# Optimization experiments

Hardware: AMD Instinct MI355X
Metric: run time of the kernel (lower is better)

## Reference

```python
import jax, jax.numpy as jnp
import numpy as np

SEQ = 10; NCH = 7; NNODES = 10; GH = 32; HEADS = 4; LH = 64; NUSERS = 1000

def _edges():
    e = []
    for i in range(4):
        e += [[i, 7], [7, i]]
    for i in range(4, 7):
        e += [[i, 8], [8, i]]
    e += [[7, 8], [8, 7], [7, 9], [9, 7], [8, 9], [9, 8]]
    a = np.array(e, dtype=np.int32)
    return a[:, 0], a[:, 1]

_SRC, _DST = _edges()

def gat_conv(x, W, att_src, att_dst, bias, concat):
    # x: [B,N,Fin], W: [Fin,H,C], att_*: [H,C]. PyG GATConv: adds self-loops, leaky_relu(0.2), edge-softmax by dst.
    src = jnp.concatenate([jnp.asarray(_SRC), jnp.arange(NNODES, dtype=jnp.int32)])
    dst = jnp.concatenate([jnp.asarray(_DST), jnp.arange(NNODES, dtype=jnp.int32)])
    xh = jnp.einsum('bnf,fhc->bnhc', x, W)            # [B,N,H,C]
    a_s = (xh * att_src).sum(-1)                       # [B,N,H]
    a_d = (xh * att_dst).sum(-1)
    e = jax.nn.leaky_relu(a_s[:, src] + a_d[:, dst], 0.2)  # [B,E,H]
    B = x.shape[0]
    m = jnp.full((B, NNODES, e.shape[-1]), -jnp.inf, e.dtype).at[:, dst].max(e)
    p = jnp.exp(e - m[:, dst])
    den = jnp.zeros((B, NNODES, e.shape[-1]), e.dtype).at[:, dst].add(p)
    alpha = p / den[:, dst]                            # softmax over incoming edges
    out = jnp.zeros(xh.shape, xh.dtype).at[:, dst].add(alpha[..., None] * xh[:, src])
    out = out.reshape(B, NNODES, -1) if concat else out.mean(axis=2)
    return out + bias

def graph_conv(x, W_rel, b_rel, W_root):
    # PyG GraphConv(aggr='add'): lin_rel(sum_{j->i} x_j) + lin_root(x_i); no self-loops.
    src = jnp.asarray(_SRC); dst = jnp.asarray(_DST)
    agg = jnp.zeros_like(x).at[:, dst].add(x[:, src])
    return agg @ W_rel + b_rel + x @ W_root

def lstm_dir(x, Wih, Whh, b):
    B, T, _ = x.shape
    H = Whh.shape[1]
    xw = jnp.einsum('btd,gd->btg', x, Wih) + b         # precompute input projections [B,T,4H]
    def step(carry, xt):
        h, c = carry
        g = xt + h @ Whh.T
        i, f, gg, o = jnp.split(g, 4, -1)
        c = jax.nn.sigmoid(f) * c + jax.nn.sigmoid(i) * jnp.tanh(gg)
        h = jax.nn.sigmoid(o) * jnp.tanh(c)
        return (h, c), h
    z = jnp.zeros((B, H), x.dtype)
    _, hs = jax.lax.scan(step, (z, z), xw.transpose(1, 0, 2))
    return hs.transpose(1, 0, 2)

def bilstm(x, Wf, Uf, bf, Wb, Ub, bb):
    fwd = lstm_dir(x, Wf, Uf, bf)
    bwd = lstm_dir(x[:, ::-1], Wb, Ub, bb)[:, ::-1]
    return jnp.concatenate([fwd, bwd], -1)

def self_attn(O, Wa, ba):
    Q = jnp.tanh(O @ Wa.T + ba)
    a = jax.nn.softmax(jnp.einsum('bqh,bkh->bqk', Q, O), axis=-1)
    return jnp.einsum('bqk,bkh->bqh', a, O)

_SPECS = {
    'ga1_W': (SEQ, HEADS, GH), 'ga1_as': (HEADS, GH), 'ga1_ad': (HEADS, GH), 'ga1_b': (HEADS * GH,),
    'ga2_W': (HEADS * GH, 1, SEQ), 'ga2_as': (1, SEQ), 'ga2_ad': (1, SEQ), 'ga2_b': (SEQ,),
    'gp1_Wrel': (SEQ, GH), 'gp1_Wroot': (SEQ, GH), 'gp1_b': (GH,),
    'gp2_Wrel': (GH, SEQ), 'gp2_Wroot': (GH, SEQ), 'gp2_b': (SEQ,),
    'l1f_Wih': (4 * LH, 3 * NCH), 'l1f_Whh': (4 * LH, LH), 'l1f_b': (4 * LH,),
    'l1b_Wih': (4 * LH, 3 * NCH), 'l1b_Whh': (4 * LH, LH), 'l1b_b': (4 * LH,),
    'l2f_Wih': (4 * LH, 2 * LH), 'l2f_Whh': (4 * LH, LH), 'l2f_b': (4 * LH,),
    'l2b_Wih': (4 * LH, 2 * LH), 'l2b_Whh': (4 * LH, LH), 'l2b_b': (4 * LH,),
    'a1_Wa': (2 * LH, 2 * LH), 'a1_ba': (2 * LH,),
    'a2_Wa': (2 * LH, 2 * LH), 'a2_ba': (2 * LH,),
    'fc_W': (NUSERS, 2 * LH), 'fc_b': (NUSERS,),
}

def setup_inputs() -> dict:
    key = jax.random.key(0)
    B = 32768
    keys = jax.random.split(key, len(_SPECS) + 1)
    inp = {'M': jax.random.normal(keys[0], (B, NCH, SEQ), dtype=jnp.float32)}
    for k, (name, shp) in zip(keys[1:], _SPECS.items()):
        inp[name] = (jax.random.normal(k, shp, dtype=jnp.float32) * 0.1)
    return inp

def reference(M, ga1_W, ga1_as, ga1_ad, ga1_b, ga2_W, ga2_as, ga2_ad, ga2_b,
              gp1_Wrel, gp1_Wroot, gp1_b, gp2_Wrel, gp2_Wroot, gp2_b,
              l1f_Wih, l1f_Whh, l1f_b, l1b_Wih, l1b_Whh, l1b_b,
              l2f_Wih, l2f_Whh, l2f_b, l2b_Wih, l2b_Whh, l2b_b,
              a1_Wa, a1_ba, a2_Wa, a2_ba, fc_W, fc_b):
    B = M.shape[0]
    pad = jnp.zeros((B, NNODES - NCH, SEQ), M.dtype)
    nf = jnp.concatenate([M, pad], axis=1)             # [B,10,10]
    h = jax.nn.relu(gat_conv(nf, ga1_W, ga1_as, ga1_ad, ga1_b, True))
    Mp = gat_conv(h, ga2_W, ga2_as, ga2_ad, ga2_b, False)[:, :NCH]
    g = jax.nn.relu(graph_conv(nf, gp1_Wrel, gp1_b, gp1_Wroot))
    bfeat = graph_conv(g, gp2_Wrel, gp2_b, gp2_Wroot)[:, :NCH]
    x = jnp.concatenate([M.transpose(0, 2, 1), Mp.transpose(0, 2, 1), bfeat.transpose(0, 2, 1)], axis=2)
    x = bilstm(x, l1f_Wih, l1f_Whh, l1f_b, l1b_Wih, l1b_Whh, l1b_b)
    x = self_attn(x, a1_Wa, a1_ba)
    x = bilstm(x, l2f_Wih, l2f_Whh, l2f_b, l2b_Wih, l2b_Whh, l2b_b)
    x = self_attn(x, a2_Wa, a2_ba)
    x = x.mean(axis=1)
    return x @ fc_W.T + fc_b
```

## Files before the change

kernel.cpp:

```cpp
#include <hip/hip_runtime.h>
#include <hip/hip_bf16.h>
#include <cstdint>


#define NCH 7
#define SEQ 10
#define NN  10

__constant__ int c_src[20] = {0,7,1,7,2,7,3,7,4,8,5,8,6,8,7,8,7,9,8,9};
__constant__ int c_dst[20] = {7,0,7,1,7,2,7,3,8,4,8,5,8,6,8,7,9,7,9,8};
__constant__ int c_in_start[11] = {0,2,4,6,8,10,12,14,21,27,30};
__constant__ int c_in_edge[30] = {1,20, 3,21, 5,22, 7,23, 9,24, 11,25, 13,26,
                                  0,2,4,6,15,17,27,
                                  8,10,12,14,19,28,
                                  16,18,29};
__constant__ int c_gin_start[11] = {0,1,2,3,4,5,6,7,13,18,20};
__constant__ int c_gin_src[20] = {7,7,7,7,8,8,8, 0,1,2,3,8,9, 4,5,6,7,9, 7,8};

__device__ __forceinline__ float fsig(float x){ return 1.f/(1.f + __expf(-x)); }
__device__ __forceinline__ float ftanh(float x){ return 1.f - 2.f/(__expf(2.f*x) + 1.f); }

typedef _Float16 h2v __attribute__((ext_vector_type(2)));
typedef _Float16 f16x4 __attribute__((ext_vector_type(4)));
typedef float    f32x4 __attribute__((ext_vector_type(4)));

#if defined(__has_builtin)
#if __has_builtin(__builtin_amdgcn_fdot2)
#define HAS_FDOT2 1
#endif
#endif

__device__ __forceinline__ float d2(uint32_t a, uint32_t b, float c){
#ifdef HAS_FDOT2
    return __builtin_amdgcn_fdot2(__builtin_bit_cast(h2v, a),
                                  __builtin_bit_cast(h2v, b), c, false);
#else
    union { uint32_t u; _Float16 h[2]; } ua, ub;
    ua.u = a; ub.u = b;
    return c + (float)ua.h[0]*(float)ub.h[0] + (float)ua.h[1]*(float)ub.h[1];
#endif
}

__device__ __forceinline__ f32x4 mfma16(f16x4 a, f16x4 b, f32x4 c){
    return __builtin_amdgcn_mfma_f32_16x16x16f16(a, b, c, 0, 0, 0);
}
__device__ __forceinline__ f16x4 ld4h(const _Float16* p){
    return __builtin_bit_cast(f16x4, *(const uint2*)(p));
}
__device__ __forceinline__ f16x4 ld4hg(const uint32_t* p){
    return __builtin_bit_cast(f16x4, *(const uint2*)(p));
}
__device__ __forceinline__ uint32_t pk2(float a, float b){
    union { _Float16 h[2]; uint32_t u; } x;
    x.h[0] = (_Float16)a; x.h[1] = (_Float16)b; return x.u;
}
__device__ __forceinline__ float2 upk2(uint32_t u){
    union { uint32_t u; _Float16 h[2]; } x; x.u = u;
    return make_float2((float)x.h[0], (float)x.h[1]);
}
#define SBAR() __builtin_amdgcn_sched_barrier(0)

#define IH1O 0
#define HH1O 8192
#define IH2O 24576
#define HH2O 57344
#define WA1O 73728
#define WA2O 81920
#define WPK_TOTAL 90112

__global__ __launch_bounds__(256) void prep_kernel(
    const float* __restrict__ w1f, const float* __restrict__ w1b,
    const float* __restrict__ h1f, const float* __restrict__ h1b,
    const float* __restrict__ w2f, const float* __restrict__ w2b,
    const float* __restrict__ h2f, const float* __restrict__ h2b,
    const float* __restrict__ wa1, const float* __restrict__ wa2,
    uint32_t* __restrict__ wpk)
{
    int i = blockIdx.x * 256 + threadIdx.x;
    if (i >= WPK_TOTAL) return;
    float v0, v1;
    if (i < 73728) {
        const float *sa, *sb; int K, NKT, base;
        if (i < 8192)       { base = 0;     NKT = 2; K = 21;  sa = w1f; sb = w1b; }
        else if (i < 24576) { base = 8192;  NKT = 4; K = 64;  sa = h1f; sb = h1b; }
        else if (i < 57344) { base = 24576; NKT = 8; K = 128; sa = w2f; sb = w2b; }
        else                { base = 57344; NKT = 4; K = 64;  sa = h2f; sb = h2b; }
        int local = i - base;
        int dsz = 16 * NKT * 128;
        const float* src = sa;
        if (local >= dsz) { src = sb; local -= dsz; }
        int entry = local >> 7;
        int lane  = (local & 127) >> 1;
        int j     = local & 1;
        int tau = entry / NKT, kt = entry - tau * NKT;
        int row = 16 * tau + (lane & 15);
        int kb  = kt * 16 + 4 * (lane >> 4) + 2 * j;
        v0 = (kb     < K) ? src[row * K + kb]     : 0.f;
        v1 = (kb + 1 < K) ? src[row * K + kb + 1] : 0.f;
    } else {
        int local = i - 73728;
        const float* src = wa1;
        if (local >= 8192) { src = wa2; local -= 8192; }
        int row = local >> 6, p = local & 63;
        int d0 = 2 * p;
        v0 = src[row * 128 + d0];
        v1 = src[row * 128 + d0 + 1];
    }
    union { _Float16 h[2]; uint32_t u; } x;
    x.h[0] = (_Float16)v0; x.h[1] = (_Float16)v1;
    wpk[i] = x.u;
}

__global__ __launch_bounds__(64) void graph_kernel(
    const float* __restrict__ M,
    const float* __restrict__ W1, const float* __restrict__ as1,
    const float* __restrict__ ad1, const float* __restrict__ b1,
    const float* __restrict__ W2, const float* __restrict__ as2,
    const float* __restrict__ ad2, const float* __restrict__ b2,
    const float* __restrict__ gWrel1, const float* __restrict__ gWroot1,
    const float* __restrict__ gb1,
    const float* __restrict__ gWrel2, const float* __restrict__ gWroot2,
    const float* __restrict__ gb2,
    float* __restrict__ xseq)
{
    const int b = blockIdx.x;
    const int tid = threadIdx.x;

    __shared__ float    s_nf[10][10];
    __shared__ uint32_t s_xhp[10][64];
    __shared__ uint32_t s_hp[10][64];
    __shared__ uint32_t s_w2p[10][64];
    __shared__ uint32_t s_a1p[64], s_d1p[64];
    __shared__ float s_as[10][4], s_ad[10][4];
    __shared__ float s_al[30][4];
    __shared__ float s_xh2[10][10];
    __shared__ float s_as2[10], s_ad2[10];
    __shared__ float s_al2[30];
    __shared__ float s_mp[10][10];
    __shared__ float s_agg[10][10];
    __shared__ float s_g[10][33];
    __shared__ float s_gagg[10][33];
    __shared__ float s_bf[10][10];

    const float* Mb = M + (size_t)b * 70;
    for (int i = tid; i < 100; i += 64) {
        int n = i / 10, f = i - n * 10;
        s_nf[n][f] = (n < 7) ? Mb[n * 10 + f] : 0.f;
    }
    s_a1p[tid] = pk2(as1[2 * tid], as1[2 * tid + 1]);
    s_d1p[tid] = pk2(ad1[2 * tid], ad1[2 * tid + 1]);
    for (int i = tid; i < 640; i += 64) {
        int c = i >> 6, j = i & 63;
        s_w2p[c][j] = pk2(W2[(2 * j) * 10 + c], W2[(2 * j + 1) * 10 + c]);
    }
    float2 w1r[10];
    #pragma unroll
    for (int f = 0; f < 10; f++)
        w1r[f] = *(const float2*)(W1 + f * 128 + 2 * tid);
    SBAR();

    #pragma unroll
    for (int n = 0; n < 10; n++) {
        float a0 = 0.f, a1 = 0.f;
        #pragma unroll
        for (int f = 0; f < 10; f++) {
            float x = s_nf[n][f];
            a0 += x * w1r[f].x; a1 += x * w1r[f].y;
        }
        s_xhp[n][tid] = pk2(a0, a1);
    }
    SBAR();

    if (tid < 40) {
        int n = tid >> 2, h = tid & 3;
        float va = 0.f, vd = 0.f;
        #pragma unroll
        for (int cp = 0; cp < 16; cp++) {
            uint32_t x = s_xhp[n][h * 16 + cp];
            va = d2(x, s_a1p[h * 16 + cp], va);
            vd = d2(x, s_d1p[h * 16 + cp], vd);
        }
        s_as[n][h] = va; s_ad[n][h] = vd;
    }
    SBAR();

    for (int i = tid; i < 120; i += 64) {
        int e = i >> 2, h = i & 3;
        int sn = (e < 20) ? c_src[e] : e - 20;
        int dn = (e < 20) ? c_dst[e] : e - 20;
        float v = s_as[sn][h] + s_ad[dn][h];
        s_al[e][h] = (v >= 0.f) ? v : 0.2f * v;
    }
    SBAR();

    if (tid < 40) {
        int n = tid >> 2, h = tid & 3;
        int st = c_in_start[n], en = c_in_start[n+1];
        float m = -1e30f;
        for (int j = st; j < en; j++) m = fmaxf(m, s_al[c_in_edge[j]][h]);
        float den = 0.f;
        for (int j = st; j < en; j++) den += __expf(s_al[c_in_edge[j]][h] - m);
        float inv = 1.f / den;
        for (int j = st; j < en; j++) {
            int e = c_in_edge[j];
            s_al[e][h] = __expf(s_al[e][h] - m) * inv;
        }
    }
    SBAR();

    for (int i = tid; i < 640; i += 64) {
        int n = i >> 6, p = i & 63;
        int h = p >> 4;
        int st = c_in_start[n], en = c_in_start[n+1];
        float2 bb = *(const float2*)(b1 + 2 * p);
        float o0 = bb.x, o1 = bb.y;
        for (int j = st; j < en; j++) {
            int e = c_in_edge[j];
            int sn = (e < 20) ? c_src[e] : e - 20;
            float al = s_al[e][h];
            float2 xf = upk2(s_xhp[sn][p]);
            o0 += al * xf.x; o1 += al * xf.y;
        }
        s_hp[n][p] = pk2(fmaxf(o0, 0.f), fmaxf(o1, 0.f));
    }
    SBAR();

    for (int i = tid; i < 100; i += 64) {
        int n = i / 10, c = i - (i / 10) * 10;
        float a = 0.f;
        #pragma unroll 16
        for (int j = 0; j < 64; j++)
            a = d2(s_hp[n][j], s_w2p[c][j], a);
        s_xh2[n][c] = a;
    }
    SBAR();

    if (tid < 20) {
        int n = (tid < 10) ? tid : tid - 10;
        const float* av = (tid < 10) ? as2 : ad2;
        float v = 0.f;
        #pragma unroll
        for (int c = 0; c < 10; c++) v += s_xh2[n][c] * av[c];
        if (tid < 10) s_as2[n] = v; else s_ad2[n] = v;
    }
    SBAR();
    if (tid < 30) {
        int e = tid;
        int sn = (e < 20) ? c_src[e] : e - 20;
        int dn = (e < 20) ? c_dst[e] : e - 20;
        float v = s_as2[sn] + s_ad2[dn];
        s_al2[e] = (v >= 0.f) ? v : 0.2f * v;
    }
    SBAR();
    if (tid < 10) {
        int st = c_in_start[tid], en = c_in_start[tid+1];
        float m = -1e30f;
        for (int j = st; j < en; j++) m = fmaxf(m, s_al2[c_in_edge[j]]);
        float den = 0.f;
        for (int j = st; j < en; j++) den += __expf(s_al2[c_in_edge[j]] - m);
        float inv = 1.f / den;
        for (int j = st; j < en; j++) s_al2[c_in_edge[j]] = __expf(s_al2[c_in_edge[j]] - m) * inv;
    }
    SBAR();
    for (int i = tid; i < 100; i += 64) {
        int n = i / 10, c = i - (i / 10) * 10;
        int st = c_in_start[n], en = c_in_start[n+1];
        float o = b2[c];
        for (int j = st; j < en; j++) {
            int e = c_in_edge[j];
            int sn = (e < 20) ? c_src[e] : e - 20;
            o += s_al2[e] * s_xh2[sn][c];
        }
        s_mp[n][c] = o;
    }
    SBAR();

    for (int i = tid; i < 100; i += 64) {
        int n = i / 10, f = i - (i / 10) * 10;
        int st = c_gin_start[n], en = c_gin_start[n+1];
        float a = 0.f;
        for (int j = st; j < en; j++) a += s_nf[c_gin_src[j]][f];
        s_agg[n][f] = a;
    }
    SBAR();
    for (int i = tid; i < 320; i += 64) {
        int n = i >> 5, c = i & 31;
        float v = gb1[c];
        #pragma unroll
        for (int f = 0; f < 10; f++)
            v += s_agg[n][f] * gWrel1[f*32 + c] + s_nf[n][f] * gWroot1[f*32 + c];
        s_g[n][c] = fmaxf(v, 0.f);
    }
    SBAR();
    for (int i = tid; i < 320; i += 64) {
        int n = i >> 5, c = i & 31;
        int st = c_gin_start[n], en = c_gin_start[n+1];
        float a = 0.f;
        for (int j = st; j < en; j++) a += s_g[c_gin_src[j]][c];
        s_gagg[n][c] = a;
    }
    SBAR();
    for (int i = tid; i < 100; i += 64) {
        int n = i / 10, c = i - (i / 10) * 10;
        float v = gb2[c];
        #pragma unroll
        for (int f = 0; f < 32; f++)
            v += s_gagg[n][f] * gWrel2[f*10 + c] + s_g[n][f] * gWroot2[f*10 + c];
        s_bf[n][c] = v;
    }
    SBAR();

    float* xo = xseq + (size_t)b * 210;
    for (int i = tid; i < 210; i += 64) {
        int t = i / 21, k = i - (i / 21) * 21;
        float v;
        if (k < 7)       v = s_nf[k][t];
        else if (k < 14) v = s_mp[k - 7][t];
        else             v = s_bf[k - 14][t];
        xo[i] = v;
    }
}


template<int L>
__device__ __forceinline__ void rec_layer(
    const uint32_t* __restrict__ wpk,
    const float* __restrict__ bf, const float* __restrict__ bb,
    uint32_t* __restrict__ sR1, uint32_t* __restrict__ sO2,
    uint32_t* __restrict__ sH, int w, int l)
{
    constexpr int NKT = (L == 1) ? 2 : 8;
    const uint32_t* bih = wpk + ((L == 1) ? IH1O : IH2O);
    const uint32_t* bhh = wpk + ((L == 1) ? HH1O : HH2O);
    const int dir = w >> 1;
    const int ub  = (w & 1) * 2;
    bih += dir * 16 * NKT * 128;
    bhh += dir * 16 * 4 * 128;
    const float* bias = dir ? bb : bf;
    const int ln = l & 15, lg = l >> 4;
    const int arow = l & 7, asub = 4 * lg;
    float bv[2][4];
    #pragma unroll
    for (int up = 0; up < 2; ++up)
        #pragma unroll
        for (int g = 0; g < 4; ++g)
            bv[up][g] = bias[64 * g + 16 * (ub + up) + ln];
    float cs[2][4] = {{0.f,0.f,0.f,0.f},{0.f,0.f,0.f,0.f}};
    const _Float16* Axh = (const _Float16*)sR1;
    _Float16* Hh  = (_Float16*)sH;
    _Float16* O2h = (_Float16*)sO2;
    for (int ss = 0; ss < 10; ++ss) {
        const int t = dir ? 9 - ss : ss;
        const int cur = ss & 1;
        f16x4 ax[NKT];
        #pragma unroll
        for (int kt = 0; kt < NKT; ++kt) {
            const int fo = (L == 1) ? (arow * 360 + t * 36 + kt * 16 + asub)
                                    : (arow * 1360 + t * 136 + kt * 16 + asub);
            ax[kt] = ld4h(Axh + fo);
        }
        f16x4 ah[4];
        #pragma unroll
        for (int kt = 0; kt < 4; ++kt)
            ah[kt] = ld4h(Hh + ((dir * 2 + cur) * 8 + arow) * 72 + kt * 16 + asub);
        #pragma unroll
        for (int up = 0; up < 2; ++up) {
            const int v = ub + up;
            f32x4 G[4];
            #pragma unroll
            for (int g = 0; g < 4; ++g) {
                const int tau = 4 * g + v;
                f32x4 c = { bv[up][g], bv[up][g], bv[up][g], bv[up][g] };
                #pragma unroll
                for (int kt = 0; kt < NKT; ++kt)
                    c = mfma16(ax[kt], ld4hg(bih + (tau * NKT + kt) * 128 + 2 * l), c);
                #pragma unroll
                for (int kt = 0; kt < 4; ++kt)
                    c = mfma16(ah[kt], ld4hg(bhh + (tau * 4 + kt) * 128 + 2 * l), c);
                G[g] = c;
            }
            if (l < 32) {
                #pragma unroll
                for (int r = 0; r < 4; ++r) {
                    const int s = asub + r;
                    const float ig = fsig(G[0][r]), fg = fsig(G[1][r]);
                    const float gg = ftanh(G[2][r]), og = fsig(G[3][r]);
                    const float c2 = fg * cs[up][r] + ig * gg;
                    cs[up][r] = c2;
                    const float hv = og * ftanh(c2);
                    const int u = 16 * v + ln;
                    Hh[((dir * 2 + (1 - cur)) * 8 + s) * 72 + u] = (_Float16)hv;
                    O2h[s * 1360 + t * 136 + dir * 64 + u] = (_Float16)hv;
                }
            }
        }
        __syncthreads();
    }
}

__device__ __forceinline__ void attn_one(
    const uint32_t* __restrict__ wa, const float* __restrict__ ba,
    uint32_t* __restrict__ sR1, const uint32_t* __restrict__ sO2,
    float* __restrict__ sSC, int l, int s, float* __restrict__ outg)
{
    const uint32_t* O2s = sO2 + s * 680;
    uint32_t* Q2s = sR1 + s * 680;
    float* sc = sSC + s * 104;

    float qa0[10], qa1[10];
    {
        float b0 = ba[l], b1 = ba[64 + l];
        #pragma unroll
        for (int t = 0; t < 10; t++) { qa0[t] = b0; qa1[t] = b1; }
    }
    #pragma unroll 4
    for (int c = 0; c < 16; c++) {
        uint4 w0 = *(const uint4*)(wa + l * 64 + c * 4);
        uint4 w1 = *(const uint4*)(wa + (64 + l) * 64 + c * 4);
        #pragma unroll
        for (int t = 0; t < 10; t++) {
            uint4 o = *(const uint4*)(O2s + t * 68 + c * 4);
            qa0[t] = d2(w0.w, o.w, d2(w0.z, o.z, d2(w0.y, o.y, d2(w0.x, o.x, qa0[t]))));
            qa1[t] = d2(w1.w, o.w, d2(w1.z, o.z, d2(w1.y, o.y, d2(w1.x, o.x, qa1[t]))));
        }
    }
    _Float16* q2h = (_Float16*)Q2s;
    #pragma unroll
    for (int t = 0; t < 10; t++) {
        q2h[t * 136 + l]      = (_Float16)ftanh(qa0[t]);
        q2h[t * 136 + 64 + l] = (_Float16)ftanh(qa1[t]);
    }
    #pragma unroll
    for (int r = 0; r < 2; r++) {
        int idx = l + r * 64;
        if (idx < 100) {
            int q = idx / 10, k = idx - 10 * q;
            float sv = 0.f;
            #pragma unroll
            for (int m = 0; m < 16; m++) {
                uint4 a = *(const uint4*)(Q2s + q * 68 + m * 4);
                uint4 b = *(const uint4*)(O2s + k * 68 + m * 4);
                sv = d2(a.w, b.w, d2(a.z, b.z, d2(a.y, b.y, d2(a.x, b.x, sv))));
            }
            sc[idx] = sv;
        }
    }
    if (l < 10) {
        float m = -1e30f;
        #pragma unroll
        for (int k = 0; k < 10; k++) m = fmaxf(m, sc[l * 10 + k]);
        float den = 0.f, e[10];
        #pragma unroll
        for (int k = 0; k < 10; k++) { e[k] = __expf(sc[l * 10 + k] - m); den += e[k]; }
        float inv = 1.f / den;
        #pragma unroll
        for (int k = 0; k < 10; k++) sc[l * 10 + k] = e[k] * inv;
    }
    float of0[10], of1[10];
    {
        const _Float16* o2h = (const _Float16*)O2s;
        #pragma unroll
        for (int k = 0; k < 10; k++) {
            of0[k] = (float)o2h[k * 136 + l];
            of1[k] = (float)o2h[k * 136 + 64 + l];
        }
    }
    float pa0[10], pa1[10];
    #pragma unroll
    for (int t = 0; t < 10; t++) { pa0[t] = 0.f; pa1[t] = 0.f; }
    #pragma unroll
    for (int k = 0; k < 10; k++) {
        float o0 = of0[k], o1 = of1[k];
        #pragma unroll
        for (int t = 0; t < 10; t++) {
            float sv = sc[t * 10 + k];
            pa0[t] += sv * o0; pa1[t] += sv * o1;
        }
    }
    if (outg) {
        float s0 = 0.f, s1 = 0.f;
        #pragma unroll
        for (int t = 0; t < 10; t++) { s0 += pa0[t]; s1 += pa1[t]; }
        outg[l] = s0 * 0.1f; outg[64 + l] = s1 * 0.1f;
    } else {
        _Float16* a2h = (_Float16*)Q2s;
        #pragma unroll
        for (int t = 0; t < 10; t++) {
            a2h[t * 136 + l]      = (_Float16)pa0[t];
            a2h[t * 136 + 64 + l] = (_Float16)pa1[t];
        }
    }
}

__global__ __launch_bounds__(256) void seq_kernel(
    const float* __restrict__ xseq, const uint32_t* __restrict__ wpk,
    const float* __restrict__ b1f, const float* __restrict__ b1b,
    const float* __restrict__ b2f, const float* __restrict__ b2b,
    const float* __restrict__ ba1, const float* __restrict__ ba2,
    float* __restrict__ xbar)
{
    __shared__ __align__(16) uint32_t sR1[8 * 680];
    __shared__ __align__(16) uint32_t sO2[8 * 680];
    __shared__ __align__(16) float    sSC[8 * 104];
    __shared__ __align__(16) uint32_t sH[1152];
    const int tid = threadIdx.x;
    const int w = tid >> 6, l = tid & 63;
    const int b0 = blockIdx.x * 8;

    {
        _Float16* xh = (_Float16*)sR1;
        const float* xs = xseq + (size_t)b0 * 210;
        for (int i = tid; i < 2880; i += 256) {
            int s = i / 360, r = i - s * 360;
            int t = r / 36, k = r - t * 36;
            float v = (k < 21) ? xs[s * 210 + t * 21 + k] : 0.f;
            xh[s * 360 + t * 36 + k] = (_Float16)v;
        }
    }
    for (int i = tid; i < 1152; i += 256) sH[i] = 0;
    __syncthreads();

    rec_layer<1>(wpk, b1f, b1b, sR1, sO2, sH, w, l);

    for (int smp = 0; smp < 2; ++smp)
        attn_one(wpk + WA1O, ba1, sR1, sO2, sSC, l, 2 * w + smp, nullptr);
    __syncthreads();
    for (int i = tid; i < 1152; i += 256) sH[i] = 0;
    __syncthreads();

    rec_layer<2>(wpk, b2f, b2b, sR1, sO2, sH, w, l);

    for (int smp = 0; smp < 2; ++smp) {
        int s = 2 * w + smp;
        attn_one(wpk + WA2O, ba2, sR1, sO2, sSC, l, s,
                 xbar + (size_t)(b0 + s) * 128);
    }
}

__global__ __launch_bounds__(256) void fc_kernel(
    const float* __restrict__ xbar, const float* __restrict__ W,
    const float* __restrict__ fb, float* __restrict__ out, int B)
{
    __shared__ __align__(16) float s_xb[64 * 132];
    const int tid = threadIdx.x;
    const int b0 = blockIdx.y * 64;
    const int u0 = blockIdx.x * 64;

    for (int i = tid; i < 64 * 128; i += 256) {
        int s = i >> 7, k = i & 127;
        int bb = b0 + s;
        s_xb[s * 132 + k] = (bb < B) ? xbar[(size_t)bb * 128 + k] : 0.f;
    }
    __syncthreads();

    const int tx = tid & 15, ty = tid >> 4;
    float acc[4][4] = {};
    for (int k = 0; k < 128; k += 4) {
        float4 wv[4], xv[4];
        #pragma unroll
        for (int j = 0; j < 4; j++) {
            int u = u0 + tx + 16 * j;
            int uc = (u < 1000) ? u : 999;
            wv[j] = *(const float4*)(W + (size_t)uc * 128 + k);
        }
        #pragma unroll
        for (int si = 0; si < 4; si++) {
            int s = ty + 16 * si;
            xv[si] = *(const float4*)(s_xb + s * 132 + k);
        }
        #pragma unroll
        for (int j = 0; j < 4; j++)
            #pragma unroll
            for (int si = 0; si < 4; si++)
                acc[j][si] += wv[j].x*xv[si].x + wv[j].y*xv[si].y
                            + wv[j].z*xv[si].z + wv[j].w*xv[si].w;
    }
    #pragma unroll
    for (int j = 0; j < 4; j++) {
        int u = u0 + tx + 16 * j;
        if (u < 1000) {
            float bb = fb[u];
            #pragma unroll
            for (int si = 0; si < 4; si++) {
                int bsm = b0 + ty + 16 * si;
                if (bsm < B) out[(size_t)bsm * 1000 + u] = acc[j][si] + bb;
            }
        }
    }
}

extern "C" void kernel_launch(void* const* d_in, const int* in_sizes, int n_in,
                              void* d_out, int out_size, void* d_ws, size_t ws_size,
                              hipStream_t stream)
{
    const float* M       = (const float*)d_in[0];
    const float* ga1_W   = (const float*)d_in[1];
    const float* ga1_as  = (const float*)d_in[2];
    const float* ga1_ad  = (const float*)d_in[3];
    const float* ga1_b   = (const float*)d_in[4];
    const float* ga2_W   = (const float*)d_in[5];
    const float* ga2_as  = (const float*)d_in[6];
    const float* ga2_ad  = (const float*)d_in[7];
    const float* ga2_b   = (const float*)d_in[8];
    const float* gp1_Wrel  = (const float*)d_in[9];
    const float* gp1_Wroot = (const float*)d_in[10];
    const float* gp1_b     = (const float*)d_in[11];
    const float* gp2_Wrel  = (const float*)d_in[12];
    const float* gp2_Wroot = (const float*)d_in[13];
    const float* gp2_b     = (const float*)d_in[14];
    const float* l1f_Wih = (const float*)d_in[15];
    const float* l1f_Whh = (const float*)d_in[16];
    const float* l1f_b   = (const float*)d_in[17];
    const float* l1b_Wih = (const float*)d_in[18];
    const float* l1b_Whh = (const float*)d_in[19];
    const float* l1b_b   = (const float*)d_in[20];
    const float* l2f_Wih = (const float*)d_in[21];
    const float* l2f_Whh = (const float*)d_in[22];
    const float* l2f_b   = (const float*)d_in[23];
    const float* l2b_Wih = (const float*)d_in[24];
    const float* l2b_Whh = (const float*)d_in[25];
    const float* l2b_b   = (const float*)d_in[26];
    const float* a1_Wa   = (const float*)d_in[27];
    const float* a1_ba   = (const float*)d_in[28];
    const float* a2_Wa   = (const float*)d_in[29];
    const float* a2_ba   = (const float*)d_in[30];
    const float* fc_W    = (const float*)d_in[31];
    const float* fc_b    = (const float*)d_in[32];

    const int B = in_sizes[0] / 70;

    float* xseq = (float*)d_ws;
    float* xbar = (float*)((char*)d_ws + (size_t)B * 210 * 4);
    uint32_t* wpk = (uint32_t*)((char*)d_ws + (size_t)B * 210 * 4
                                            + (size_t)B * 128 * 4);

    prep_kernel<<<(WPK_TOTAL + 255) / 256, 256, 0, stream>>>(
        l1f_Wih, l1b_Wih, l1f_Whh, l1b_Whh,
        l2f_Wih, l2b_Wih, l2f_Whh, l2b_Whh,
        a1_Wa, a2_Wa, wpk);

    graph_kernel<<<B, 64, 0, stream>>>(M,
        ga1_W, ga1_as, ga1_ad, ga1_b,
        ga2_W, ga2_as, ga2_ad, ga2_b,
        gp1_Wrel, gp1_Wroot, gp1_b,
        gp2_Wrel, gp2_Wroot, gp2_b,
        xseq);

    seq_kernel<<<B / 8, 256, 0, stream>>>(xseq, wpk,
        l1f_b, l1b_b, l2f_b, l2b_b, a1_ba, a2_ba, xbar);

    dim3 fgrid((1000 + 63) / 64, (B + 63) / 64);
    fc_kernel<<<fgrid, 256, 0, stream>>>(xbar, fc_W, fc_b, (float*)d_out, B);
}
```

Before: 2.408 ms.

## Process four samples per block in graph kernel with shared-memory staged weights

The graph kernel now runs 256-thread blocks where each 64-lane wave handles one batch sample, using a per-wave workspace struct in LDS. Weights, biases and graph topology tables are loaded once per block into shared memory instead of per-sample global or constant reads. This is meant to cut redundant weight loads and launch/scheduling overhead from many tiny blocks. It increases LDS use per block and assumes the batch size divides by four.

```diff
diff --git a/kernel.cpp b/kernel.cpp
--- a/kernel.cpp
+++ b/kernel.cpp
@@ -111,7 +111,22 @@
     wpk[i] = x.u;
 }
 
-__global__ __launch_bounds__(64) void graph_kernel(
+struct GWk {
+    float    nf[10][10];
+    uint32_t xhp[10][64];
+    uint32_t hp[10][64];
+    float    as_[10][4], ad_[10][4];
+    float    al[30][4];
+    float    xh2[10][10];
+    float    as2[10], ad2[10], al2[30];
+    float    mp[10][10];
+    float    agg[10][10];
+    float    g[10][33];
+    float    gagg[10][33];
+    float    bf[10][10];
+};
+
+__global__ __launch_bounds__(256) void graph_kernel(
     const float* __restrict__ M,
     const float* __restrict__ W1, const float* __restrict__ as1,
     const float* __restrict__ ad1, const float* __restrict__ b1,
@@ -123,40 +138,55 @@
     const float* __restrict__ gb2,
     float* __restrict__ xseq)
 {
-    const int b = blockIdx.x;
+    __shared__ __align__(16) GWk gw[4];
+    __shared__ __align__(16) uint32_t sw2p[640];
+    __shared__ uint32_t sa1p[64], sd1p[64];
+    __shared__ float swrel1[320], swroot1[320];
+    __shared__ float swrel2[320], swroot2[320];
+    __shared__ __align__(16) float sb1[128];
+    __shared__ float sb2[12], sgb1[32], sgb2[12];
+    __shared__ int sin_start[12], sin_edge[32];
+    __shared__ int sgin_start[12], sgin_src[20], ssrc[20], sdst[20];
+
     const int tid = threadIdx.x;
-
-    __shared__ float    s_nf[10][10];
-    __shared__ uint32_t s_xhp[10][64];
-    __shared__ uint32_t s_hp[10][64];
-    __shared__ uint32_t s_w2p[10][64];
-    __shared__ uint32_t s_a1p[64], s_d1p[64];
-    __shared__ float s_as[10][4], s_ad[10][4];
-    __shared__ float s_al[30][4];
-    __shared__ float s_xh2[10][10];
-    __shared__ float s_as2[10], s_ad2[10];
-    __shared__ float s_al2[30];
-    __shared__ float s_mp[10][10];
-    __shared__ float s_agg[10][10];
-    __shared__ float s_g[10][33];
-    __shared__ float s_gagg[10][33];
-    __shared__ float s_bf[10][10];
-
+    const int wid = tid >> 6, l = tid & 63;
+    const int b = blockIdx.x * 4 + wid;
+
+    for (int i = tid; i < 640; i += 256) {
+        int c = i >> 6, j = i & 63;
+        sw2p[i] = pk2(W2[(2 * j) * 10 + c], W2[(2 * j + 1) * 10 + c]);
+    }
+    if (tid < 64)       sa1p[tid]      = pk2(as1[2 * tid], as1[2 * tid + 1]);
+    else if (tid < 128) sd1p[tid - 64] = pk2(ad1[2 * (tid - 64)], ad1[2 * (tid - 64) + 1]);
+    for (int i = tid; i < 320; i += 256) {
+        swrel1[i] = gWrel1[i]; swroot1[i] = gWroot1[i];
+        swrel2[i] = gWrel2[i]; swroot2[i] = gWroot2[i];
+    }
+    if (tid < 128) sb1[tid] = b1[tid];
+    if (tid >= 128 && tid < 138) sb2[tid - 128] = b2[tid - 128];
+    if (tid >= 144 && tid < 176) sgb1[tid - 144] = gb1[tid - 144];
+    if (tid >= 176 && tid < 186) sgb2[tid - 176] = gb2[tid - 176];
+    if (tid >= 192 && tid < 203) {
+        sin_start[tid - 192]  = c_in_start[tid - 192];
+        sgin_start[tid - 192] = c_gin_start[tid - 192];
+    }
+    if (tid >= 203 && tid < 233) sin_edge[tid - 203] = c_in_edge[tid - 203];
+    if (tid >= 233 && tid < 253) {
+        int e = tid - 233;
+        sgin_src[e] = c_gin_src[e]; ssrc[e] = c_src[e]; sdst[e] = c_dst[e];
+    }
+    __syncthreads();
+
+    GWk& Wv = gw[wid];
     const float* Mb = M + (size_t)b * 70;
-    for (int i = tid; i < 100; i += 64) {
+    for (int i = l; i < 100; i += 64) {
         int n = i / 10, f = i - n * 10;
-        s_nf[n][f] = (n < 7) ? Mb[n * 10 + f] : 0.f;
-    }
-    s_a1p[tid] = pk2(as1[2 * tid], as1[2 * tid + 1]);
-    s_d1p[tid] = pk2(ad1[2 * tid], ad1[2 * tid + 1]);
-    for (int i = tid; i < 640; i += 64) {
-        int c = i >> 6, j = i & 63;
-        s_w2p[c][j] = pk2(W2[(2 * j) * 10 + c], W2[(2 * j + 1) * 10 + c]);
+        Wv.nf[n][f] = (n < 7) ? Mb[n * 10 + f] : 0.f;
     }
     float2 w1r[10];
     #pragma unroll
     for (int f = 0; f < 10; f++)
-        w1r[f] = *(const float2*)(W1 + f * 128 + 2 * tid);
+        w1r[f] = *(const float2*)(W1 + f * 128 + 2 * l);
     SBAR();
 
     #pragma unroll
@@ -164,159 +194,160 @@
         float a0 = 0.f, a1 = 0.f;
         #pragma unroll
         for (int f = 0; f < 10; f++) {
-            float x = s_nf[n][f];
+            float x = Wv.nf[n][f];
             a0 += x * w1r[f].x; a1 += x * w1r[f].y;
         }
-        s_xhp[n][tid] = pk2(a0, a1);
-    }
-    SBAR();
-
-    if (tid < 40) {
-        int n = tid >> 2, h = tid & 3;
+        Wv.xhp[n][l] = pk2(a0, a1);
+    }
+    SBAR();
+
+    if (l < 40) {
+        int n = l >> 2, h = l & 3;
         float va = 0.f, vd = 0.f;
         #pragma unroll
         for (int cp = 0; cp < 16; cp++) {
-            uint32_t x = s_xhp[n][h * 16 + cp];
-            va = d2(x, s_a1p[h * 16 + cp], va);
-            vd = d2(x, s_d1p[h * 16 + cp], vd);
-        }
-        s_as[n][h] = va; s_ad[n][h] = vd;
-    }
-    SBAR();
-
-    for (int i = tid; i < 120; i += 64) {
+            uint32_t x = Wv.xhp[n][h * 16 + cp];
+            va = d2(x, sa1p[h * 16 + cp], va);
+            vd = d2(x, sd1p[h * 16 + cp], vd);
+        }
+        Wv.as_[n][h] = va; Wv.ad_[n][h] = vd;
+    }
+    SBAR();
+
+    for (int i = l; i < 120; i += 64) {
         int e = i >> 2, h = i & 3;
-        int sn = (e < 20) ? c_src[e] : e - 20;
-        int dn = (e < 20) ? c_dst[e] : e - 20;
-        float v = s_as[sn][h] + s_ad[dn][h];
-        s_al[e][h] = (v >= 0.f) ? v : 0.2f * v;
-    }
-    SBAR();
-
-    if (tid < 40) {
-        int n = tid >> 2, h = tid & 3;
-        int st = c_in_start[n], en = c_in_start[n+1];
+        int sn = (e < 20) ? ssrc[e] : e - 20;
+        int dn = (e < 20) ? sdst[e] : e - 20;
+        float v = Wv.as_[sn][h] + Wv.ad_[dn][h];
+        Wv.al[e][h] = (v >= 0.f) ? v : 0.2f * v;
+    }
+    SBAR();
+
+    if (l < 40) {
+        int n = l >> 2, h = l & 3;
+        int st = sin_start[n], en = sin_start[n + 1];
         float m = -1e30f;
-        for (int j = st; j < en; j++) m = fmaxf(m, s_al[c_in_edge[j]][h]);
+        for (int j = st; j < en; j++) m = fmaxf(m, Wv.al[sin_edge[j]][h]);
         float den = 0.f;
-        for (int j = st; j < en; j++) den += __expf(s_al[c_in_edge[j]][h] - m);
+        for (int j = st; j < en; j++) den += __expf(Wv.al[sin_edge[j]][h] - m);
         float inv = 1.f / den;
         for (int j = st; j < en; j++) {
-            int e = c_in_edge[j];
-            s_al[e][h] = __expf(s_al[e][h] - m) * inv;
-        }
-    }
-    SBAR();
-
-    for (int i = tid; i < 640; i += 64) {
+            int e = sin_edge[j];
+            Wv.al[e][h] = __expf(Wv.al[e][h] - m) * inv;
+        }
+    }
+    SBAR();
+
+    for (int i = l; i < 640; i += 64) {
         int n = i >> 6, p = i & 63;
         int h = p >> 4;
-        int st = c_in_start[n], en = c_in_start[n+1];
-        float2 bb = *(const float2*)(b1 + 2 * p);
-        float o0 = bb.x, o1 = bb.y;
+        int st = sin_start[n], en = sin_start[n + 1];
+        float o0 = sb1[2 * p], o1 = sb1[2 * p + 1];
         for (int j = st; j < en; j++) {
-            int e = c_in_edge[j];
-            int sn = (e < 20) ? c_src[e] : e - 20;
-            float al = s_al[e][h];
-            float2 xf = upk2(s_xhp[sn][p]);
+            int e = sin_edge[j];
+            int sn = (e < 20) ? ssrc[e] : e - 20;
+            float al = Wv.al[e][h];
+            float2 xf = upk2(Wv.xhp[sn][p]);
             o0 += al * xf.x; o1 += al * xf.y;
         }
-        s_hp[n][p] = pk2(fmaxf(o0, 0.f), fmaxf(o1, 0.f));
-    }
-    SBAR();
-
-    for (int i = tid; i < 100; i += 64) {
+        Wv.hp[n][p] = pk2(fmaxf(o0, 0.f), fmaxf(o1, 0.f));
+    }
+    SBAR();
+
+    for (int i = l; i < 100; i += 64) {
         int n = i / 10, c = i - (i / 10) * 10;
+        float a0 = 0.f, a1 = 0.f;
+        #pragma unroll 8
+        for (int j = 0; j < 64; j += 2) {
+            a0 = d2(Wv.hp[n][j],     sw2p[c * 64 + j],     a0);
+            a1 = d2(Wv.hp[n][j + 1], sw2p[c * 64 + j + 1], a1);
+        }
+        Wv.xh2[n][c] = a0 + a1;
+    }
+    SBAR();
+
+    if (l < 20) {
+        int n = (l < 10) ? l : l - 10;
+        const float* av = (l < 10) ? as2 : ad2;
+        float v = 0.f;
+        #pragma unroll
+        for (int c = 0; c < 10; c++) v += Wv.xh2[n][c] * av[c];
+        if (l < 10) Wv.as2[n] = v; else Wv.ad2[n] = v;
+    }
+    SBAR();
+    if (l < 30) {
+        int e = l;
+        int sn = (e < 20) ? ssrc[e] : e - 20;
+        int dn = (e < 20) ? sdst[e] : e - 20;
+        float v = Wv.as2[sn] + Wv.ad2[dn];
+        Wv.al2[e] = (v >= 0.f) ? v : 0.2f * v;
+    }
+    SBAR();
+    if (l < 10) {
+        int st = sin_start[l], en = sin_start[l + 1];
+        float m = -1e30f;
+        for (int j = st; j < en; j++) m = fmaxf(m, Wv.al2[sin_edge[j]]);
+        float den = 0.f;
+        for (int j = st; j < en; j++) den += __expf(Wv.al2[sin_edge[j]] - m);
+        float inv = 1.f / den;
+        for (int j = st; j < en; j++) Wv.al2[sin_edge[j]] = __expf(Wv.al2[sin_edge[j]] - m) * inv;
+    }
+    SBAR();
+    for (int i = l; i < 100; i += 64) {
+        int n = i / 10, c = i - (i / 10) * 10;
+        int st = sin_start[n], en = sin_start[n + 1];
+        float o = sb2[c];
+        for (int j = st; j < en; j++) {
+            int e = sin_edge[j];
+            int sn = (e < 20) ? ssrc[e] : e - 20;
+            o += Wv.al2[e] * Wv.xh2[sn][c];
+        }
+        Wv.mp[n][c] = o;
+    }
+    SBAR();
+
+    for (int i = l; i < 100; i += 64) {
+        int n = i / 10, f = i - (i / 10) * 10;
+        int st = sgin_start[n], en = sgin_start[n + 1];
         float a = 0.f;
-        #pragma unroll 16
-        for (int j = 0; j < 64; j++)
-            a = d2(s_hp[n][j], s_w2p[c][j], a);
-        s_xh2[n][c] = a;
-    }
-    SBAR();
-
-    if (tid < 20) {
-        int n = (tid < 10) ? tid : tid - 10;
-        const float* av = (tid < 10) ? as2 : ad2;
-        float v = 0.f;
-        #pragma unroll
-        for (int c = 0; c < 10; c++) v += s_xh2[n][c] * av[c];
-        if (tid < 10) s_as2[n] = v; else s_ad2[n] = v;
-    }
-    SBAR();
-    if (tid < 30) {
-        int e = tid;
-        int sn = (e < 20) ? c_src[e] : e - 20;
-        int dn = (e < 20) ? c_dst[e] : e - 20;
-        float v = s_as2[sn] + s_ad2[dn];
-        s_al2[e] = (v >= 0.f) ? v : 0.2f * v;
-    }
-    SBAR();
-    if (tid < 10) {
-        int st = c_in_start[tid], en = c_in_start[tid+1];
-        float m = -1e30f;
-        for (int j = st; j < en; j++) m = fmaxf(m, s_al2[c_in_edge[j]]);
-        float den = 0.f;
-        for (int j = st; j < en; j++) den += __expf(s_al2[c_in_edge[j]] - m);
-        float inv = 1.f / den;
-        for (int j = st; j < en; j++) s_al2[c_in_edge[j]] = __expf(s_al2[c_in_edge[j]] - m) * inv;
-    }
-    SBAR();
-    for (int i = tid; i < 100; i += 64) {
+        for (int j = st; j < en; j++) a += Wv.nf[sgin_src[j]][f];
+        Wv.agg[n][f] = a;
+    }
+    SBAR();
+    for (int i = l; i < 320; i += 64) {
+        int n = i >> 5, c = i & 31;
+        float v = sgb1[c];
+        #pragma unroll
+        for (int f = 0; f < 10; f++)
+            v += Wv.agg[n][f] * swrel1[f * 32 + c] + Wv.nf[n][f] * swroot1[f * 32 + c];
+        Wv.g[n][c] = fmaxf(v, 0.f);
+    }
+    SBAR();
+    for (int i = l; i < 320; i += 64) {
+        int n = i >> 5, c = i & 31;
+        int st = sgin_start[n], en = sgin_start[n + 1];
+        float a = 0.f;
+        for (int j = st; j < en; j++) a += Wv.g[sgin_src[j]][c];
+        Wv.gagg[n][c] = a;
+    }
+    SBAR();
+    for (int i = l; i < 100; i += 64) {
         int n = i / 10, c = i - (i / 10) * 10;
-        int st = c_in_start[n], en = c_in_start[n+1];
-        float o = b2[c];
-        for (int j = st; j < en; j++) {
-            int e = c_in_edge[j];
-            int sn = (e < 20) ? c_src[e] : e - 20;
-            o += s_al2[e] * s_xh2[sn][c];
-        }
-        s_mp[n][c] = o;
-    }
-    SBAR();
-
-    for (int i = tid; i < 100; i += 64) {
-        int n = i / 10, f = i - (i / 10) * 10;
-        int st = c_gin_start[n], en = c_gin_start[n+1];
-        float a = 0.f;
-        for (int j = st; j < en; j++) a += s_nf[c_gin_src[j]][f];
-        s_agg[n][f] = a;
-    }
-    SBAR();
-    for (int i = tid; i < 320; i += 64) {
-        int n = i >> 5, c = i & 31;
-        float v = gb1[c];
-        #pragma unroll
-        for (int f = 0; f < 10; f++)
-            v += s_agg[n][f] * gWrel1[f*32 + c] + s_nf[n][f] * gWroot1[f*32 + c];
-        s_g[n][c] = fmaxf(v, 0.f);
-    }
-    SBAR();
-    for (int i = tid; i < 320; i += 64) {
-        int n = i >> 5, c = i & 31;
-        int st = c_gin_start[n], en = c_gin_start[n+1];
-        float a = 0.f;
-        for (int j = st; j < en; j++) a += s_g[c_gin_src[j]][c];
-        s_gagg[n][c] = a;
-    }
-    SBAR();
-    for (int i = tid; i < 100; i += 64) {
-        int n = i / 10, c = i - (i / 10) * 10;
-        float v = gb2[c];
+        float v = sgb2[c];
         #pragma unroll
         for (int f = 0; f < 32; f++)
-            v += s_gagg[n][f] * gWrel2[f*10 + c] + s_g[n][f] * gWroot2[f*10 + c];
-        s_bf[n][c] = v;
+            v += Wv.gagg[n][f] * swrel2[f * 10 + c] + Wv.g[n][f] * swroot2[f * 10 + c];
+        Wv.bf[n][c] = v;
     }
     SBAR();
 
     float* xo = xseq + (size_t)b * 210;
-    for (int i = tid; i < 210; i += 64) {
+    for (int i = l; i < 210; i += 64) {
         int t = i / 21, k = i - (i / 21) * 21;
         float v;
-        if (k < 7)       v = s_nf[k][t];
-        else if (k < 14) v = s_mp[k - 7][t];
-        else             v = s_bf[k - 14][t];
+        if (k < 7)       v = Wv.nf[k][t];
+        else if (k < 14) v = Wv.mp[k - 7][t];
+        else             v = Wv.bf[k - 14][t];
         xo[i] = v;
     }
 }
@@ -639,7 +670,7 @@
         l2f_Wih, l2b_Wih, l2f_Whh, l2b_Whh,
         a1_Wa, a2_Wa, wpk);
 
-    graph_kernel<<<B, 64, 0, stream>>>(M,
+    graph_kernel<<<B / 4, 256, 0, stream>>>(M,
         ga1_W, ga1_as, ga1_ad, ga1_b,
         ga2_W, ga2_as, ga2_ad, ga2_b,
         gp1_Wrel, gp1_Wroot, gp1_b,
```

Measured after the change: 2.307 ms. -4.2%, faster.
